# Kernel optimization log

Hardware: AMD Instinct MI355X
Metric: run time of the kernel (lower is better)

## Reference

```python
import jax, jax.numpy as jnp
import numpy as np

K = 7          # involution kernel size
PAD = (K - 1) // 2
EPS = 1e-5     # BatchNorm eps (torch default)


def setup_inputs() -> dict:
    key = jax.random.key(0)
    ks = jax.random.split(key, 5)
    B, C, H, W = 4, 128, 64, 64
    Cr = C // 4
    x = jax.random.normal(ks[0], (B, C, H, W), dtype=jnp.float32)
    w1 = jax.random.normal(ks[1], (Cr, C), dtype=jnp.float32) * (1.0 / np.sqrt(C))
    b1 = jax.random.normal(ks[2], (Cr,), dtype=jnp.float32) * 0.01
    bn_gamma = jnp.ones((Cr,), dtype=jnp.float32)
    bn_beta = jnp.zeros((Cr,), dtype=jnp.float32)
    bn_mean = jnp.zeros((Cr,), dtype=jnp.float32)
    bn_var = jnp.ones((Cr,), dtype=jnp.float32)
    w2 = jax.random.normal(ks[3], (K * K, Cr), dtype=jnp.float32) * (1.0 / np.sqrt(Cr))
    b2 = jax.random.normal(ks[4], (K * K,), dtype=jnp.float32) * 0.01
    return {"x": x, "w1": w1, "b1": b1, "bn_gamma": bn_gamma, "bn_beta": bn_beta,
            "bn_mean": bn_mean, "bn_var": bn_var, "w2": w2, "b2": b2}


def _gen_kernel(x, w1, b1, bn_gamma, bn_beta, bn_mean, bn_var, w2, b2):
    # 1x1 conv -> BN (eval mode, running stats) -> ReLU -> 1x1 conv
    f = jnp.einsum('oc,bchw->bohw', w1, x) + b1[None, :, None, None]
    scale = bn_gamma / jnp.sqrt(bn_var + EPS)
    f = f * scale[None, :, None, None] + (bn_beta - bn_mean * scale)[None, :, None, None]
    f = jax.nn.relu(f)
    return jnp.einsum('oc,bchw->bohw', w2, f) + b2[None, :, None, None]  # [B, K*K, H, W]


def reference(x, w1, b1, bn_gamma, bn_beta, bn_mean, bn_var, w2, b2):
    B, C, H, W = x.shape
    kernel = _gen_kernel(x, w1, b1, bn_gamma, bn_beta, bn_mean, bn_var, w2, b2)
    xp = jnp.pad(x, ((0, 0), (0, 0), (PAD, PAD), (PAD, PAD)))
    # Fused unfold-multiply-sum: accumulate over the K*K fixed offsets instead of
    # materializing the [B, C, K*K, H, W] im2col tensor.
    out = jnp.zeros_like(x)
    for i in range(K):
        for j in range(K):
            idx = i * K + j
            out = out + kernel[:, idx:idx + 1] * xp[:, :, i:i + H, j:j + W]
    return out
```

## Files before the change

kernel.cpp:

```cpp
#include <hip/hip_runtime.h>

#define KS 7
#define KK 49
#define CIN 128
#define CR 32
#define WW 64
#define HWSZ 4096

__global__ __launch_bounds__(256) void gen_kernel(
    const float* __restrict__ x, const float* __restrict__ w1,
    const float* __restrict__ b1, const float* __restrict__ bn_gamma,
    const float* __restrict__ bn_beta, const float* __restrict__ bn_mean,
    const float* __restrict__ bn_var, const float* __restrict__ w2,
    const float* __restrict__ b2, float* __restrict__ ker)
{
    __shared__ float fs[4][64][33];
    const int tid  = threadIdx.x;
    const int lane = tid & 63;
    const int q    = tid >> 6;
    const int pix  = blockIdx.x * 64 + lane;
    const int b    = pix >> 12;
    const int hw   = pix & 4095;

    const float* xp = x + ((size_t)b * CIN) * HWSZ + hw;

    float f[CR];
#pragma unroll
    for (int o = 0; o < CR; ++o) f[o] = 0.f;

    const int cbeg = q * 32;
#pragma unroll 8
    for (int ci = 0; ci < 32; ++ci) {
        const int c = cbeg + ci;
        const float xv = xp[(size_t)c * HWSZ];
#pragma unroll
        for (int o = 0; o < CR; ++o)
            f[o] += w1[o * CIN + c] * xv;
    }

#pragma unroll
    for (int o = 0; o < CR; ++o) fs[q][lane][o] = f[o];
    __syncthreads();

    float fr[CR];
#pragma unroll
    for (int o = 0; o < CR; ++o)
        fr[o] = fs[0][lane][o] + fs[1][lane][o] + fs[2][lane][o] + fs[3][lane][o];

#pragma unroll
    for (int o = 0; o < CR; ++o) {
        const float sc = bn_gamma[o] * rsqrtf(bn_var[o] + 1e-5f);
        const float v  = (fr[o] + b1[o]) * sc + (bn_beta[o] - bn_mean[o] * sc);
        fr[o] = fmaxf(v, 0.f);
    }

    const int pbeg = q * 13;
    const int pend = (pbeg + 13 < KK) ? (pbeg + 13) : KK;
    float* kout = ker + ((size_t)b * KK) * HWSZ + hw;
    for (int p = pbeg; p < pend; ++p) {
        float s = b2[p];
#pragma unroll
        for (int o = 0; o < CR; ++o)
            s += w2[p * CR + o] * fr[o];
        kout[(size_t)p * HWSZ] = s;
    }
}

__global__ __launch_bounds__(256) void inv_gather(
    const float* __restrict__ x, const float* __restrict__ ker,
    float* __restrict__ out)
{
    __shared__ float xs[2][484 * 4];

    const int bid = blockIdx.x;
    const int cs  = bid & 7;
    const int tw  = (bid >> 3) & 3;
    const int th  = (bid >> 5) & 3;
    const int b   = bid >> 7;

    const int h0 = th * 16, w0 = tw * 16, c0 = cs * 16;
    const int tid = threadIdx.x;
    const int tx = tid & 15, ty = tid >> 4;
    const int h = h0 + ty, w = w0 + tx;

    float kr[KK];
    const float* kp = ker + ((size_t)b * KK) * HWSZ + h * WW + w;
#pragma unroll
    for (int p = 0; p < KK; ++p) kr[p] = kp[(size_t)p * HWSZ];

    const size_t xbase = (size_t)b * CIN * HWSZ;
    const int spbase = ty * 22 + tx;

    auto stage = [&](int buf, int cbase) {
        for (int sp = tid; sp < 484; sp += 256) {
            const int row = sp / 22;
            const int col = sp - row * 22;
            const int gr = h0 - 3 + row;
            const int gc = w0 - 3 + col;
            float4 v = {0.f, 0.f, 0.f, 0.f};
            if ((unsigned)gr < 64u && (unsigned)gc < 64u) {
                const float* xp = &x[xbase + (size_t)cbase * HWSZ + gr * WW + gc];
                v.x = xp[0];
                v.y = xp[HWSZ];
                v.z = xp[2 * HWSZ];
                v.w = xp[3 * HWSZ];
            }
            *reinterpret_cast<float4*>(&xs[buf][sp * 4]) = v;
        }
    };

    stage(0, c0);
    __syncthreads();

    for (int cg = 0; cg < 4; ++cg) {
        const int cbase = c0 + cg * 4;
        if (cg < 3) stage((cg + 1) & 1, cbase + 4);

        float ax = 0.f, ay = 0.f, az = 0.f, aw = 0.f;
        const float* xb = &xs[cg & 1][0];
#pragma unroll
        for (int i = 0; i < KS; ++i) {
#pragma unroll
            for (int j = 0; j < KS; ++j) {
                const float4 xv = *reinterpret_cast<const float4*>(
                    &xb[(spbase + i * 22 + j) * 4]);
                const float k = kr[i * KS + j];
                ax += k * xv.x; ay += k * xv.y; az += k * xv.z; aw += k * xv.w;
            }
        }

        const size_t obase = xbase + (size_t)cbase * HWSZ + h * WW + w;
        out[obase]            = ax;
        out[obase + HWSZ]     = ay;
        out[obase + 2 * HWSZ] = az;
        out[obase + 3 * HWSZ] = aw;

        __syncthreads();
    }
}

extern "C" void kernel_launch(void* const* d_in, const int* in_sizes, int n_in,
                              void* d_out, int out_size, void* d_ws, size_t ws_size,
                              hipStream_t stream) {
    const float* x        = (const float*)d_in[0];
    const float* w1       = (const float*)d_in[1];
    const float* b1       = (const float*)d_in[2];
    const float* bn_gamma = (const float*)d_in[3];
    const float* bn_beta  = (const float*)d_in[4];
    const float* bn_mean  = (const float*)d_in[5];
    const float* bn_var   = (const float*)d_in[6];
    const float* w2       = (const float*)d_in[7];
    const float* b2       = (const float*)d_in[8];
    float* ker = (float*)d_ws;
    float* out = (float*)d_out;

    gen_kernel<<<256, 256, 0, stream>>>(x, w1, b1, bn_gamma, bn_beta,
                                        bn_mean, bn_var, w2, b2, ker);
    inv_gather<<<512, 256, 0, stream>>>(x, ker, out);
}
```

Measured before the change: 102.9 us.

## Widen gen_kernel to 512 threads and split gather into 8-channel blocks

gen_kernel now runs 8 waves per 64-pixel block, each reducing 16 input channels. The cross-wave reduction and the BN/ReLU step are split across waves and passed through float4 LDS traffic, and the 49 output taps are spread as 7/6/6/... per wave. inv_gather doubles its grid to 1024 blocks, each covering 8 channels with a single staged tile instead of a double-buffered loop over 16 channels. This is meant to raise parallelism and occupancy on both kernels. In exchange, each gather block re-reads the 49 kernel weights per pixel twice as often, and halo loads are repeated across more blocks.

After: 98.56 us. -4.3%, faster.

```diff
diff --git a/kernel.cpp b/kernel.cpp
--- a/kernel.cpp
+++ b/kernel.cpp
@@ -7,14 +7,14 @@
 #define WW 64
 #define HWSZ 4096
 
-__global__ __launch_bounds__(256) void gen_kernel(
+__global__ __launch_bounds__(512) void gen_kernel(
     const float* __restrict__ x, const float* __restrict__ w1,
     const float* __restrict__ b1, const float* __restrict__ bn_gamma,
     const float* __restrict__ bn_beta, const float* __restrict__ bn_mean,
     const float* __restrict__ bn_var, const float* __restrict__ w2,
     const float* __restrict__ b2, float* __restrict__ ker)
 {
-    __shared__ float fs[4][64][33];
+    __shared__ float fs[8][64][36];
     const int tid  = threadIdx.x;
     const int lane = tid & 63;
     const int q    = tid >> 6;
@@ -24,45 +24,67 @@
 
     const float* xp = x + ((size_t)b * CIN) * HWSZ + hw;
 
+    const float* w1q = w1 + __builtin_amdgcn_readfirstlane(q * 16);
+
     float f[CR];
 #pragma unroll
     for (int o = 0; o < CR; ++o) f[o] = 0.f;
 
-    const int cbeg = q * 32;
-#pragma unroll 8
-    for (int ci = 0; ci < 32; ++ci) {
-        const int c = cbeg + ci;
-        const float xv = xp[(size_t)c * HWSZ];
+#pragma unroll
+    for (int ci = 0; ci < 16; ++ci) {
+        const float xv = xp[(size_t)(q * 16 + ci) * HWSZ];
 #pragma unroll
         for (int o = 0; o < CR; ++o)
-            f[o] += w1[o * CIN + c] * xv;
+            f[o] += w1q[o * CIN + ci] * xv;
     }
 
 #pragma unroll
-    for (int o = 0; o < CR; ++o) fs[q][lane][o] = f[o];
+    for (int o = 0; o < CR; o += 4) {
+        float4 v = {f[o], f[o + 1], f[o + 2], f[o + 3]};
+        *reinterpret_cast<float4*>(&fs[q][lane][o]) = v;
+    }
+    __syncthreads();
+
+    const int ob = q * 4;
+    float4 r = {0.f, 0.f, 0.f, 0.f};
+#pragma unroll
+    for (int g = 0; g < 8; ++g) {
+        const float4 v = *reinterpret_cast<const float4*>(&fs[g][lane][ob]);
+        r.x += v.x; r.y += v.y; r.z += v.z; r.w += v.w;
+    }
+    {
+        float rr[4] = {r.x, r.y, r.z, r.w};
+#pragma unroll
+        for (int k = 0; k < 4; ++k) {
+            const int o = ob + k;
+            const float sc = bn_gamma[o] * rsqrtf(bn_var[o] + 1e-5f);
+            const float v  = (rr[k] + b1[o]) * sc + (bn_beta[o] - bn_mean[o] * sc);
+            rr[k] = fmaxf(v, 0.f);
+        }
+        float4 w = {rr[0], rr[1], rr[2], rr[3]};
+        *reinterpret_cast<float4*>(&fs[0][lane][ob]) = w;
+    }
     __syncthreads();
 
     float fr[CR];
 #pragma unroll
-    for (int o = 0; o < CR; ++o)
-        fr[o] = fs[0][lane][o] + fs[1][lane][o] + fs[2][lane][o] + fs[3][lane][o];
-
-#pragma unroll
-    for (int o = 0; o < CR; ++o) {
-        const float sc = bn_gamma[o] * rsqrtf(bn_var[o] + 1e-5f);
-        const float v  = (fr[o] + b1[o]) * sc + (bn_beta[o] - bn_mean[o] * sc);
-        fr[o] = fmaxf(v, 0.f);
+    for (int o = 0; o < CR; o += 4) {
+        const float4 v = *reinterpret_cast<const float4*>(&fs[0][lane][o]);
+        fr[o] = v.x; fr[o + 1] = v.y; fr[o + 2] = v.z; fr[o + 3] = v.w;
     }
 
-    const int pbeg = q * 13;
-    const int pend = (pbeg + 13 < KK) ? (pbeg + 13) : KK;
+    const int p0 = (q == 0) ? 0 : q * 6 + 1;
+    const int np = (q == 0) ? 7 : 6;
+    const float* w2q = w2 + __builtin_amdgcn_readfirstlane(p0 * CR);
     float* kout = ker + ((size_t)b * KK) * HWSZ + hw;
-    for (int p = pbeg; p < pend; ++p) {
-        float s = b2[p];
+#pragma unroll
+    for (int pi = 0; pi < 7; ++pi) {
+        if (pi >= np) break;
+        float s = b2[p0 + pi];
 #pragma unroll
         for (int o = 0; o < CR; ++o)
-            s += w2[p * CR + o] * fr[o];
-        kout[(size_t)p * HWSZ] = s;
+            s += w2q[pi * CR + o] * fr[o];
+        kout[(size_t)(p0 + pi) * HWSZ] = s;
     }
 }
 
@@ -70,15 +92,16 @@
     const float* __restrict__ x, const float* __restrict__ ker,
     float* __restrict__ out)
 {
-    __shared__ float xs[2][484 * 4];
+    __shared__ float xsA[484 * 4];
+    __shared__ float xsB[484 * 4];
 
     const int bid = blockIdx.x;
-    const int cs  = bid & 7;
-    const int tw  = (bid >> 3) & 3;
-    const int th  = (bid >> 5) & 3;
-    const int b   = bid >> 7;
+    const int cs  = bid & 15;
+    const int tw  = (bid >> 4) & 3;
+    const int th  = (bid >> 6) & 3;
+    const int b   = bid >> 8;
 
-    const int h0 = th * 16, w0 = tw * 16, c0 = cs * 16;
+    const int h0 = th * 16, w0 = tw * 16, c0 = cs * 8;
     const int tid = threadIdx.x;
     const int tx = tid & 15, ty = tid >> 4;
     const int h = h0 + ty, w = w0 + tx;
@@ -88,55 +111,53 @@
 #pragma unroll
     for (int p = 0; p < KK; ++p) kr[p] = kp[(size_t)p * HWSZ];
 
-    const size_t xbase = (size_t)b * CIN * HWSZ;
-    const int spbase = ty * 22 + tx;
+    const size_t xbase = (size_t)b * CIN * HWSZ + (size_t)c0 * HWSZ;
 
-    auto stage = [&](int buf, int cbase) {
-        for (int sp = tid; sp < 484; sp += 256) {
-            const int row = sp / 22;
-            const int col = sp - row * 22;
-            const int gr = h0 - 3 + row;
-            const int gc = w0 - 3 + col;
-            float4 v = {0.f, 0.f, 0.f, 0.f};
-            if ((unsigned)gr < 64u && (unsigned)gc < 64u) {
-                const float* xp = &x[xbase + (size_t)cbase * HWSZ + gr * WW + gc];
-                v.x = xp[0];
-                v.y = xp[HWSZ];
-                v.z = xp[2 * HWSZ];
-                v.w = xp[3 * HWSZ];
-            }
-            *reinterpret_cast<float4*>(&xs[buf][sp * 4]) = v;
+    for (int e = tid; e < 968; e += 256) {
+        const int sp   = e >> 1;
+        const int half = e & 1;
+        const int row = sp / 22;
+        const int col = sp - row * 22;
+        const int gr = h0 - 3 + row;
+        const int gc = w0 - 3 + col;
+        float4 v = {0.f, 0.f, 0.f, 0.f};
+        if ((unsigned)gr < 64u && (unsigned)gc < 64u) {
+            const float* xp = &x[xbase + (size_t)(half * 4) * HWSZ + gr * WW + gc];
+            v.x = xp[0];
+            v.y = xp[HWSZ];
+            v.z = xp[2 * HWSZ];
+            v.w = xp[3 * HWSZ];
         }
-    };
-
-    stage(0, c0);
+        float* dst = half ? xsB : xsA;
+        *reinterpret_cast<float4*>(&dst[sp * 4]) = v;
+    }
     __syncthreads();
 
-    for (int cg = 0; cg < 4; ++cg) {
-        const int cbase = c0 + cg * 4;
-        if (cg < 3) stage((cg + 1) & 1, cbase + 4);
+    float a0 = 0.f, a1 = 0.f, a2 = 0.f, a3 = 0.f;
+    float a4 = 0.f, a5 = 0.f, a6 = 0.f, a7 = 0.f;
+    const int spbase = ty * 22 + tx;
+#pragma unroll
+    for (int i = 0; i < KS; ++i) {
+#pragma unroll
+        for (int j = 0; j < KS; ++j) {
+            const int sp = spbase + i * 22 + j;
+            const float k = kr[i * KS + j];
+            const float4 va = *reinterpret_cast<const float4*>(&xsA[sp * 4]);
+            const float4 vb = *reinterpret_cast<const float4*>(&xsB[sp * 4]);
+            a0 += k * va.x; a1 += k * va.y; a2 += k * va.z; a3 += k * va.w;
+            a4 += k * vb.x; a5 += k * vb.y; a6 += k * vb.z; a7 += k * vb.w;
+        }
+    }
 
-        float ax = 0.f, ay = 0.f, az = 0.f, aw = 0.f;
-        const float* xb = &xs[cg & 1][0];
-#pragma unroll
-        for (int i = 0; i < KS; ++i) {
-#pragma unroll
-            for (int j = 0; j < KS; ++j) {
-                const float4 xv = *reinterpret_cast<const float4*>(
-                    &xb[(spbase + i * 22 + j) * 4]);
-                const float k = kr[i * KS + j];
-                ax += k * xv.x; ay += k * xv.y; az += k * xv.z; aw += k * xv.w;
-            }
-        }
-
-        const size_t obase = xbase + (size_t)cbase * HWSZ + h * WW + w;
-        out[obase]            = ax;
-        out[obase + HWSZ]     = ay;
-        out[obase + 2 * HWSZ] = az;
-        out[obase + 3 * HWSZ] = aw;
-
-        __syncthreads();
-    }
+    const size_t obase = xbase + h * WW + w;
+    out[obase]            = a0;
+    out[obase + HWSZ]     = a1;
+    out[obase + 2 * HWSZ] = a2;
+    out[obase + 3 * HWSZ] = a3;
+    out[obase + 4 * HWSZ] = a4;
+    out[obase + 5 * HWSZ] = a5;
+    out[obase + 6 * HWSZ] = a6;
+    out[obase + 7 * HWSZ] = a7;
 }
 
 extern "C" void kernel_launch(void* const* d_in, const int* in_sizes, int n_in,
@@ -154,7 +175,7 @@
     float* ker = (float*)d_ws;
     float* out = (float*)d_out;
 
-    gen_kernel<<<256, 256, 0, stream>>>(x, w1, b1, bn_gamma, bn_beta,
+    gen_kernel<<<256, 512, 0, stream>>>(x, w1, b1, bn_gamma, bn_beta,
                                         bn_mean, bn_var, w2, b2, ker);
-    inv_gather<<<512, 256, 0, stream>>>(x, ker, out);
+    inv_gather<<<1024, 256, 0, stream>>>(x, ker, out);
 }
```
